# Optimization experiments

Measured on AMD Instinct MI355X. Metric: run time of the kernel, lower is better.

## Reference

```python
import jax, jax.numpy as jnp
import numpy as np

CHANNELS = 64
STRIDE = 2


def _blur_kernel(channels, dtype):
    # fixed binomial [1,2,1]/4 separable kernel -> 3x3x3 outer product
    k1 = jnp.array([1.0, 2.0, 1.0], dtype=dtype) / 4.0
    k3 = jnp.einsum('i,j,k->ijk', k1, k1, k1)            # [3,3,3]
    # depthwise conv weight: [O=C, I/groups=1, 3,3,3]
    return jnp.broadcast_to(k3, (channels, 1, 3, 3, 3))


def setup_inputs() -> dict:
    key = jax.random.key(0)
    x = jax.random.normal(key, (4, CHANNELS, 32, 112, 112), dtype=jnp.float32)
    return {"x": x}


def reference(x):
    # replicate (edge) padding of 1 on D,H,W, matching padding_mode='replicate'
    xp = jnp.pad(x, ((0, 0), (0, 0), (1, 1), (1, 1), (1, 1)), mode='edge')
    w = _blur_kernel(x.shape[1], x.dtype)
    # grouped (depthwise) 3D conv, stride 2, VALID after explicit padding
    out = jax.lax.conv_general_dilated(
        xp, w,
        window_strides=(STRIDE, STRIDE, STRIDE),
        padding='VALID',
        dimension_numbers=('NCDHW', 'OIDHW', 'NCDHW'),
        feature_group_count=x.shape[1],
    )
    return out
```

## Files before the change

### kernel.cpp

```cpp
#include <hip/hip_runtime.h>


#define IN_D 32
#define IN_H 112
#define IN_W 112
#define OUT_D 16
#define OUT_H 56
#define OUT_W 56

__global__ __launch_bounds__(256) void blurpool3d_kernel(
    const float* __restrict__ x, float* __restrict__ out, int total)
{
    int idx = blockIdx.x * 256 + threadIdx.x;
    if (idx >= total) return;

    int ow = idx % OUT_W;
    int t  = idx / OUT_W;
    int oh = t % OUT_H;
    t /= OUT_H;
    int od = t % OUT_D;
    int nc = t / OUT_D;

    int iw1 = 2 * ow;
    int ih1 = 2 * oh;
    int id1 = 2 * od;
    int iw0 = max(iw1 - 1, 0);
    int ih0 = max(ih1 - 1, 0);
    int id0 = max(id1 - 1, 0);

    const float* p = x + (size_t)nc * (IN_D * IN_H * IN_W);

    float dsum = 0.0f;
#pragma unroll
    for (int kd = 0; kd < 3; ++kd) {
        int id = (kd == 0) ? id0 : (kd == 1 ? id1 : id1 + 1);
        const float* pd = p + (size_t)id * (IN_H * IN_W);
        float hsum = 0.0f;
#pragma unroll
        for (int kh = 0; kh < 3; ++kh) {
            int ih = (kh == 0) ? ih0 : (kh == 1 ? ih1 : ih1 + 1);
            const float* ph = pd + ih * IN_W;
            float a = ph[iw0];
            float b = ph[iw1];
            float c = ph[iw1 + 1];
            float wsum = a + 2.0f * b + c;
            hsum += (kh == 1 ? 2.0f : 1.0f) * wsum;
        }
        dsum += (kd == 1 ? 2.0f : 1.0f) * hsum;
    }
    out[idx] = dsum * (1.0f / 64.0f);
}

extern "C" void kernel_launch(void* const* d_in, const int* in_sizes, int n_in,
                              void* d_out, int out_size, void* d_ws, size_t ws_size,
                              hipStream_t stream)
{
    const float* x = (const float*)d_in[0];
    float* out = (float*)d_out;
    int total = out_size;
    int grid = (total + 255) / 256;
    blurpool3d_kernel<<<grid, 256, 0, stream>>>(x, out, total);
}
```

Before: 571.6 us.

## Compute 8x8 output tile per thread with vectorized loads and depth-plane reuse

Each thread now produces 8 consecutive W outputs across 8 consecutive D outputs. It loads rows with float4 and carries the shared depth plane's horizontal sums forward instead of reloading them. This cuts redundant global loads and index arithmetic. In exchange the grid shrinks to 784 blocks, which lowers parallelism and occupancy for latency hiding, and the grid size is hardcoded to the fixed shape.

```diff
diff --git a/kernel.cpp b/kernel.cpp
--- a/kernel.cpp
+++ b/kernel.cpp
@@ -7,48 +7,88 @@
 #define OUT_D 16
 #define OUT_H 56
 #define OUT_W 56
+#define PLANE (IN_H * IN_W)
+#define OW8 7
+#define ODH 2
+
+__device__ __forceinline__ void plane_hsum(const float* __restrict__ pd,
+                                           int ih0, int ih1, int ih2,
+                                           int iwbase, int iwl, float hs[8])
+{
+#pragma unroll
+    for (int j = 0; j < 8; ++j) hs[j] = 0.f;
+    const int ihs[3] = {ih0, ih1, ih2};
+#pragma unroll
+    for (int kh = 0; kh < 3; ++kh) {
+        const float* row = pd + ihs[kh] * IN_W;
+        float4 r0 = *(const float4*)(row + iwbase);
+        float4 r1 = *(const float4*)(row + iwbase + 4);
+        float4 r2 = *(const float4*)(row + iwbase + 8);
+        float4 r3 = *(const float4*)(row + iwbase + 12);
+        float left = row[iwl];
+        float wt = (kh == 1) ? 2.0f : 1.0f;
+        hs[0] = fmaf(wt, left + 2.f * r0.x + r0.y, hs[0]);
+        hs[1] = fmaf(wt, r0.y + 2.f * r0.z + r0.w, hs[1]);
+        hs[2] = fmaf(wt, r0.w + 2.f * r1.x + r1.y, hs[2]);
+        hs[3] = fmaf(wt, r1.y + 2.f * r1.z + r1.w, hs[3]);
+        hs[4] = fmaf(wt, r1.w + 2.f * r2.x + r2.y, hs[4]);
+        hs[5] = fmaf(wt, r2.y + 2.f * r2.z + r2.w, hs[5]);
+        hs[6] = fmaf(wt, r2.w + 2.f * r3.x + r3.y, hs[6]);
+        hs[7] = fmaf(wt, r3.y + 2.f * r3.z + r3.w, hs[7]);
+    }
+}
 
 __global__ __launch_bounds__(256) void blurpool3d_kernel(
-    const float* __restrict__ x, float* __restrict__ out, int total)
+    const float* __restrict__ x, float* __restrict__ out)
 {
     int idx = blockIdx.x * 256 + threadIdx.x;
-    if (idx >= total) return;
+    int t    = idx;
+    int ow8  = t % OW8;  t /= OW8;
+    int oh   = t % OUT_H; t /= OUT_H;
+    int odh  = t % ODH;
+    int nc   = t / ODH;
 
-    int ow = idx % OUT_W;
-    int t  = idx / OUT_W;
-    int oh = t % OUT_H;
-    t /= OUT_H;
-    int od = t % OUT_D;
-    int nc = t / OUT_D;
+    int iwbase = ow8 * 16;
+    int iwl    = max(iwbase - 1, 0);
+    int ih1 = 2 * oh;
+    int ih0 = max(ih1 - 1, 0);
+    int ih2 = ih1 + 1;
+    int od0 = odh * 8;
 
-    int iw1 = 2 * ow;
-    int ih1 = 2 * oh;
-    int id1 = 2 * od;
-    int iw0 = max(iw1 - 1, 0);
-    int ih0 = max(ih1 - 1, 0);
-    int id0 = max(id1 - 1, 0);
+    const float* p = x + (size_t)nc * (IN_D * PLANE);
 
-    const float* p = x + (size_t)nc * (IN_D * IN_H * IN_W);
+    float hprev[8];
+    {
+        int id = max(2 * od0 - 1, 0);
+        plane_hsum(p + (size_t)id * PLANE, ih0, ih1, ih2, iwbase, iwl, hprev);
+    }
 
-    float dsum = 0.0f;
+    size_t obase = (((size_t)nc * OUT_D + od0) * OUT_H + oh) * OUT_W + ow8 * 8;
+
 #pragma unroll
-    for (int kd = 0; kd < 3; ++kd) {
-        int id = (kd == 0) ? id0 : (kd == 1 ? id1 : id1 + 1);
-        const float* pd = p + (size_t)id * (IN_H * IN_W);
-        float hsum = 0.0f;
+    for (int k = 0; k < 8; ++k) {
+        int od = od0 + k;
+        float h1[8], h2[8];
+        plane_hsum(p + (size_t)(2 * od) * PLANE,     ih0, ih1, ih2, iwbase, iwl, h1);
+        plane_hsum(p + (size_t)(2 * od + 1) * PLANE, ih0, ih1, ih2, iwbase, iwl, h2);
+
+        float4 o0, o1;
+        o0.x = (hprev[0] + 2.f * h1[0] + h2[0]) * (1.f / 64.f);
+        o0.y = (hprev[1] + 2.f * h1[1] + h2[1]) * (1.f / 64.f);
+        o0.z = (hprev[2] + 2.f * h1[2] + h2[2]) * (1.f / 64.f);
+        o0.w = (hprev[3] + 2.f * h1[3] + h2[3]) * (1.f / 64.f);
+        o1.x = (hprev[4] + 2.f * h1[4] + h2[4]) * (1.f / 64.f);
+        o1.y = (hprev[5] + 2.f * h1[5] + h2[5]) * (1.f / 64.f);
+        o1.z = (hprev[6] + 2.f * h1[6] + h2[6]) * (1.f / 64.f);
+        o1.w = (hprev[7] + 2.f * h1[7] + h2[7]) * (1.f / 64.f);
+
+        float* o = out + obase + (size_t)k * (OUT_H * OUT_W);
+        *(float4*)o = o0;
+        *(float4*)(o + 4) = o1;
+
 #pragma unroll
-        for (int kh = 0; kh < 3; ++kh) {
-            int ih = (kh == 0) ? ih0 : (kh == 1 ? ih1 : ih1 + 1);
-            const float* ph = pd + ih * IN_W;
-            float a = ph[iw0];
-            float b = ph[iw1];
-            float c = ph[iw1 + 1];
-            float wsum = a + 2.0f * b + c;
-            hsum += (kh == 1 ? 2.0f : 1.0f) * wsum;
-        }
-        dsum += (kd == 1 ? 2.0f : 1.0f) * hsum;
+        for (int j = 0; j < 8; ++j) hprev[j] = h2[j];
     }
-    out[idx] = dsum * (1.0f / 64.0f);
 }
 
 extern "C" void kernel_launch(void* const* d_in, const int* in_sizes, int n_in,
@@ -57,7 +97,5 @@
 {
     const float* x = (const float*)d_in[0];
     float* out = (float*)d_out;
-    int total = out_size;
-    int grid = (total + 255) / 256;
-    blurpool3d_kernel<<<grid, 256, 0, stream>>>(x, out, total);
+    blurpool3d_kernel<<<784, 256, 0, stream>>>(x, out);
 }
```

Measured after the change: 642.2 us. 1.12x slower.
